# Kernel tuning notes

Hardware: AMD Instinct MI355X
Metric: run time of the kernel (lower is better)

The kernel has to match this reference:

```python
import jax, jax.numpy as jnp
import numpy as np

N = 50000; E = 800000; NFEAT = 128; NHID = 64; CONCAT = 2; NCLASS = 40
D = CONCAT * NHID
BN_EPS = 1e-5


def setup_inputs() -> dict:
    key = jax.random.key(0)
    ks = jax.random.split(key, 16)
    rn = lambda k, s, sc=0.05: jax.random.normal(k, s, jnp.float32) * sc
    return {
        "x1a": rn(ks[0], (N, NFEAT), 1.0),
        "x1b": rn(ks[1], (N, NFEAT), 1.0),
        "x2a": rn(ks[2], (N, NFEAT), 1.0),
        "x2b": rn(ks[3], (N, NFEAT), 1.0),
        "edge_index1": jax.random.randint(ks[4], (2, E), 0, N),
        "edge_index2": jax.random.randint(ks[5], (2, E), 0, N),
        "Wi": rn(ks[6], (CONCAT, NFEAT, NHID)),
        "bi": jnp.zeros((CONCAT, NHID), jnp.float32),
        "gi": jnp.ones((CONCAT, NHID), jnp.float32),
        "bei": jnp.zeros((CONCAT, NHID), jnp.float32),
        "Wm": rn(ks[7], (2, D, D)),
        "bm": jnp.zeros((2, D), jnp.float32),
        "gm": jnp.ones((2, D), jnp.float32),
        "bem": jnp.zeros((2, D), jnp.float32),
        "Wf": rn(ks[8], (D, NCLASS)),
        "bf": jnp.zeros((NCLASS,), jnp.float32),
        "fc1w1_W": rn(ks[9], (D,)),
        "fc1w1_b": jnp.zeros((1,), jnp.float32),
        "fc1w2_W": rn(ks[10], (D,)),
        "fc1w2_b": jnp.zeros((1,), jnp.float32),
        "aws_w1_W": rn(ks[11], (2, D)),
        "aws_w1_b": jnp.zeros((2,), jnp.float32),
        "aws_w2_W": rn(ks[12], (2, D)),
        "aws_w2_b": jnp.zeros((2,), jnp.float32),
        "fcw1_W": rn(ks[13], (NCLASS,)),
        "fcw1_b": jnp.zeros((1,), jnp.float32),
        "fcw2_W": rn(ks[14], (NCLASS,)),
        "fcw2_b": jnp.zeros((1,), jnp.float32),
    }


def _gcn_norm(edge_index, n):
    # GCN symmetric normalization with self-loops (cached=True behaviour)
    loop = jnp.arange(n)
    src = jnp.concatenate([edge_index[0], loop])
    dst = jnp.concatenate([edge_index[1], loop])
    deg = jax.ops.segment_sum(jnp.ones_like(dst, jnp.float32), dst, n)
    dinv = jnp.where(deg > 0, deg ** -0.5, 0.0)
    return src, dst, dinv[src] * dinv[dst]


def _gcn(x, W, b, g):
    # GCNConv: dense projection then sparse scatter-based aggregation
    src, dst, norm = g
    h = x @ W
    agg = jax.ops.segment_sum(h[src] * norm[:, None], dst, x.shape[0])
    return agg + b


def _bn(x, gamma, beta):
    m = x.mean(0)
    v = jnp.mean((x - m) ** 2, axis=0)
    return (x - m) * jax.lax.rsqrt(v + BN_EPS) * gamma + beta


def _gate(x1, x2, w1, b1, w2, b2):
    # sigmoid gates L1-normalized; only the last node's row is used (w[-1,:])
    s1 = jax.nn.sigmoid(jnp.dot(x1[-1], w1) + b1)
    s2 = jax.nn.sigmoid(jnp.dot(x2[-1], w2) + b2)
    t = s1 + s2
    return s1 / t, s2 / t


def _forward(x1a, x1b, x2a, x2b, g1, g2, Wi, bi, gi, bei, Wm, bm, gm, bem,
             Wf, bf, fc1w1_W, fc1w1_b, fc1w2_W, fc1w2_b,
             aws_w1_W, aws_w1_b, aws_w2_W, aws_w2_b,
             fcw1_W, fcw1_b, fcw2_W, fcw2_b):
    xs1, xs2 = (x1a, x1b), (x2a, x2b)
    h1 = jnp.concatenate([jax.nn.relu(_bn(_gcn(xs1[i], Wi[i], bi[i], g1), gi[i], bei[i]))
                          for i in range(CONCAT)], axis=-1)
    h2 = jnp.concatenate([jax.nn.relu(_bn(_gcn(xs2[i], Wi[i], bi[i], g2), gi[i], bei[i]))
                          for i in range(CONCAT)], axis=-1)
    w1, w2 = _gate(h1, h2, fc1w1_W, fc1w1_b[0], fc1w2_W, fc1w2_b[0])
    x = w1 * h1 + w2 * h2
    for i in range(Wm.shape[0]):  # middle layers (n_layers - 2)
        a = jax.nn.relu(_bn(_gcn(x, Wm[i], bm[i], g1), gm[i], bem[i]))
        b = jax.nn.relu(_bn(_gcn(x, Wm[i], bm[i], g2), gm[i], bem[i]))
        w1, w2 = _gate(a, b, aws_w1_W[i], aws_w1_b[i], aws_w2_W[i], aws_w2_b[i])
        x = w1 * a + w2 * b
    p1 = _gcn(x, Wf, bf, g1)
    p2 = _gcn(x, Wf, bf, g2)
    w1, w2 = _gate(p1, p2, fcw1_W, fcw1_b[0], fcw2_W, fcw2_b[0])
    return (w1 * p1 + w2 * p2, p1, p2)


def reference(x1a, x1b, x2a, x2b, edge_index1, edge_index2, Wi, bi, gi, bei,
              Wm, bm, gm, bem, Wf, bf, fc1w1_W, fc1w1_b, fc1w2_W, fc1w2_b,
              aws_w1_W, aws_w1_b, aws_w2_W, aws_w2_b,
              fcw1_W, fcw1_b, fcw2_W, fcw2_b):
    g1 = _gcn_norm(edge_index1, N)
    g2 = _gcn_norm(edge_index2, N)
    return _forward(x1a, x1b, x2a, x2b, g1, g2, Wi, bi, gi, bei, Wm, bm, gm, bem,
                    Wf, bf, fc1w1_W, fc1w1_b, fc1w2_W, fc1w2_b,
                    aws_w1_W, aws_w1_b, aws_w2_W, aws_w2_b,
                    fcw1_W, fcw1_b, fcw2_W, fcw2_b)
```

## Files before the change

### kernel.cpp

```cpp
#include <hip/hip_runtime.h>
#include <hip/hip_fp16.h>


#define DFEAT 128

typedef __attribute__((ext_vector_type(8))) short bf16x8;
typedef __attribute__((ext_vector_type(4))) float f32x4;

__device__ __forceinline__ unsigned short f2bf(float f) {
    unsigned u = __float_as_uint(f);
    u += 0x7fffu + ((u >> 16) & 1u);
    return (unsigned short)(u >> 16);
}
__device__ __forceinline__ float bf2f(unsigned short u) {
    return __uint_as_float((unsigned)u << 16);
}
__device__ __forceinline__ float4 bf4tof4(ushort4 u) {
    return make_float4(__uint_as_float((unsigned)u.x << 16),
                       __uint_as_float((unsigned)u.y << 16),
                       __uint_as_float((unsigned)u.z << 16),
                       __uint_as_float((unsigned)u.w << 16));
}
__device__ __forceinline__ unsigned f2h16(float f) {
    return (unsigned)__half_as_ushort(__float2half(f));
}
__device__ __forceinline__ float h16f(unsigned u) {
    return __half2float(__ushort_as_half((unsigned short)u));
}

constexpr int RSH = 13;
constexpr int RSZ = 8192;
constexpr int NRMAX = 8;
constexpr int EPA = 2048;
constexpr int SUBS = 16;
constexpr int SCAP = 160000;

__global__ __launch_bounds__(256) void partA_kernel(
    const int* __restrict__ src1, const int* __restrict__ dst1,
    const int* __restrict__ src2, const int* __restrict__ dst2,
    int* __restrict__ stg, int* __restrict__ gcount, int E, int nr) {
    int g = blockIdx.y;
    const int* src = g ? src2 : src1;
    const int* dst = g ? dst2 : dst1;
    __shared__ int buf[EPA];
    __shared__ int buf2[EPA];
    __shared__ int cnt8[NRMAX + 1], pre8[NRMAX + 1], base8[NRMAX];
    int t = threadIdx.x;
    if (t < NRMAX) cnt8[t] = 0;
    __syncthreads();
    int e0 = blockIdx.x * EPA;
    int e1 = min(e0 + EPA, E);
    int ec = e1 - e0;
    for (int i = e0 + t; i < e1; i += 256) {
        int d = dst[i];
        int s = src[i];
        buf[i - e0] = (d << 16) | s;
        atomicAdd(&cnt8[d >> RSH], 1);
    }
    __syncthreads();
    if (t == 0) {
        int run = 0;
        for (int r = 0; r < nr; ++r) { pre8[r] = run; run += cnt8[r]; }
        pre8[nr] = run;
    }
    __syncthreads();
    if (t < nr) {
        base8[t] = atomicAdd(&gcount[g * NRMAX + t], cnt8[t]);
        cnt8[t] = 0;
    }
    __syncthreads();
    for (int j = t; j < ec; j += 256) {
        int v = buf[j];
        int d = (unsigned)v >> 16;
        int r = d >> RSH;
        int p = pre8[r] + atomicAdd(&cnt8[r], 1);
        buf2[p] = ((d & (RSZ - 1)) << 16) | (v & 0xFFFF);
    }
    __syncthreads();
    for (int j = t; j < ec; j += 256) {
        int r = 0;
        while (j >= pre8[r + 1]) ++r;
        int gpos = base8[r] + (j - pre8[r]);
        if (gpos < SCAP) stg[((size_t)g * NRMAX + r) * SCAP + gpos] = buf2[j];
    }
}

__global__ __launch_bounds__(256) void histB_kernel(
    const int* __restrict__ stg, const int* __restrict__ gcount,
    int* __restrict__ baseB, int nr) {
    int g = blockIdx.y;
    int r = blockIdx.x / SUBS;
    int sub = blockIdx.x % SUBS;
    __shared__ int hist[RSZ];
    int t = threadIdx.x;
    for (int i = t; i < RSZ; i += 256) hist[i] = 0;
    __syncthreads();
    int len = min(gcount[g * NRMAX + r], SCAP);
    int seg = (len + SUBS - 1) / SUBS;
    int e0 = sub * seg, e1 = min(e0 + seg, len);
    const int* sp = stg + ((size_t)g * NRMAX + r) * SCAP;
    for (int i = e0 + t; i < e1; i += 256) atomicAdd(&hist[(unsigned)sp[i] >> 16], 1);
    __syncthreads();
    int* bp = baseB + (((size_t)(g * NRMAX + r) * SUBS + sub) << RSH);
    for (int i = t; i < RSZ; i += 256) bp[i] = hist[i];
}

__global__ __launch_bounds__(256) void scanB_kernel(
    int* __restrict__ baseB, int* __restrict__ cnt1, int* __restrict__ cnt2, int n) {
    int node = blockIdx.x * 256 + threadIdx.x;
    int g = blockIdx.y;
    if (node >= n) return;
    int r = node >> RSH, dloc = node & (RSZ - 1);
    int* p = baseB + (((size_t)(g * NRMAX + r) * SUBS) << RSH) + dloc;
    int run = 0;
#pragma unroll
    for (int s = 0; s < SUBS; ++s) {
        int v = p[(size_t)s << RSH];
        p[(size_t)s << RSH] = run;
        run += v;
    }
    (g ? cnt2 : cnt1)[node] = run;
}

__global__ __launch_bounds__(256) void fillC_kernel(
    const int* __restrict__ stg, const int* __restrict__ gcount,
    const int* __restrict__ baseB,
    const int* __restrict__ rp1, const int* __restrict__ rp2,
    const float* __restrict__ dv1, const float* __restrict__ dv2,
    int* __restrict__ cs1, int* __restrict__ cs2, int n, int nr) {
    int g = blockIdx.y;
    int r = blockIdx.x / SUBS;
    int sub = blockIdx.x % SUBS;
    const int* rp = g ? rp2 : rp1;
    const float* dv = g ? dv2 : dv1;
    int* cs = g ? cs2 : cs1;
    __shared__ int off[RSZ];
    int t = threadIdx.x;
    int r0 = r << RSH;
    int rn = min(RSZ, n - r0);
    if (rn <= 0) return;
    const int* bp = baseB + (((size_t)(g * NRMAX + r) * SUBS + sub) << RSH);
    for (int i = t; i < rn; i += 256) off[i] = bp[i] + rp[r0 + i];
    __syncthreads();
    int len = min(gcount[g * NRMAX + r], SCAP);
    int seg = (len + SUBS - 1) / SUBS;
    int e0 = sub * seg, e1 = min(e0 + seg, len);
    const int* sp = stg + ((size_t)g * NRMAX + r) * SCAP;
    for (int i = e0 + t; i < e1; i += 256) {
        int v = sp[i];
        int dloc = (unsigned)v >> 16;
        int s = v & 0xFFFF;
        float w = dv[r0 + dloc] * dv[s];
        int pos = atomicAdd(&off[dloc], 1);
        cs[pos] = (int)((f2h16(w) << 16) | (unsigned)s);
    }
}

__global__ __launch_bounds__(256) void blocksum_kernel(const int* __restrict__ c1,
                                                       const int* __restrict__ c2,
                                                       int* __restrict__ bs, int n, int nb) {
    const int* c = blockIdx.y ? c2 : c1;
    int* out = bs + (size_t)blockIdx.y * nb;
    int t = threadIdx.x;
    int base = blockIdx.x * 2048 + t * 8;
    int s = 0;
#pragma unroll
    for (int i = 0; i < 8; ++i) {
        int idx = base + i;
        if (idx < n) s += c[idx];
    }
    __shared__ int red[256];
    red[t] = s;
    __syncthreads();
    for (int o = 128; o > 0; o >>= 1) {
        if (t < o) red[t] += red[t + o];
        __syncthreads();
    }
    if (t == 0) out[blockIdx.x] = red[0];
}

__global__ void scansums_kernel(int* __restrict__ bs, int nb, int* __restrict__ rp1,
                                int* __restrict__ rp2, int n, int E, float* __restrict__ stats) {
    int t = threadIdx.x;
    if (t < 2) {
        int* b = bs + (size_t)t * nb;
        int run = 0;
        for (int i = 0; i < nb; ++i) {
            int v = b[i];
            b[i] = run;
            run += v;
        }
        (t ? rp2 : rp1)[n] = E;
    }
    for (int i = t; i < 512; i += 64) stats[i] = 0.f;
}

__global__ __launch_bounds__(256) void writerp_kernel(const int* __restrict__ c1,
                                                      const int* __restrict__ c2,
                                                      const int* __restrict__ bs,
                                                      int* __restrict__ rp1, int* __restrict__ rp2,
                                                      float* __restrict__ dv1,
                                                      float* __restrict__ dv2, int n, int nb) {
    const int* c = blockIdx.y ? c2 : c1;
    int* rp = blockIdx.y ? rp2 : rp1;
    float* dv = blockIdx.y ? dv2 : dv1;
    int boff = bs[(size_t)blockIdx.y * nb + blockIdx.x];
    int t = threadIdx.x;
    int base = blockIdx.x * 2048 + t * 8;
    int v[8];
    int s = 0;
#pragma unroll
    for (int i = 0; i < 8; ++i) {
        int idx = base + i;
        v[i] = (idx < n) ? c[idx] : 0;
        s += v[i];
    }
    __shared__ int red[256];
    red[t] = s;
    __syncthreads();
    for (int o = 1; o < 256; o <<= 1) {
        int x = (t >= o) ? red[t - o] : 0;
        __syncthreads();
        red[t] += x;
        __syncthreads();
    }
    int run = boff + red[t] - s;
#pragma unroll
    for (int i = 0; i < 8; ++i) {
        int idx = base + i;
        if (idx < n) {
            rp[idx] = run;
            dv[idx] = rsqrtf((float)(v[i] + 1));
            run += v[i];
        }
    }
}

template <int FV, typename OutT>
__global__ __launch_bounds__(256) void dualagg_kernel(
    const unsigned short* __restrict__ h1, const unsigned short* __restrict__ h2,
    const int* __restrict__ rp1, const int* __restrict__ cs1, const float* __restrict__ dv1,
    const int* __restrict__ rp2, const int* __restrict__ cs2, const float* __restrict__ dv2,
    const float* __restrict__ bias, OutT* __restrict__ o1, OutT* __restrict__ o2, int n) {
    constexpr int COLS = FV * 4;
    const unsigned short* h;
    const int *rp, *cs;
    const float* dv;
    OutT* out;
    if (blockIdx.y == 0) { h = h1; rp = rp1; cs = cs1; dv = dv1; out = o1; }
    else                 { h = h2; rp = rp2; cs = cs2; dv = dv2; out = o2; }
    int wid = blockIdx.x * 4 + (threadIdx.x >> 6);
    if (wid >= n) return;
    int lane = threadIdx.x & 63;
    int half = lane >> 5;
    int l = lane & 31;
    bool act = (l < FV);
    float4 acc = make_float4(0.f, 0.f, 0.f, 0.f);
    int e0 = rp[wid], e1 = rp[wid + 1];
    int e = e0 + half;
    for (; e + 6 < e1; e += 8) {
        int va = cs[e], vb = cs[e + 2], vc = cs[e + 4], vd = cs[e + 6];
        float wa = h16f((unsigned)va >> 16); int sa = va & 0xFFFF;
        float wb = h16f((unsigned)vb >> 16); int sb = vb & 0xFFFF;
        float wc = h16f((unsigned)vc >> 16); int sc = vc & 0xFFFF;
        float wd = h16f((unsigned)vd >> 16); int sd = vd & 0xFFFF;
        if (act) {
            float4 ha = bf4tof4(((const ushort4*)(h + (size_t)sa * COLS))[l]);
            float4 hb = bf4tof4(((const ushort4*)(h + (size_t)sb * COLS))[l]);
            float4 hc = bf4tof4(((const ushort4*)(h + (size_t)sc * COLS))[l]);
            float4 hd = bf4tof4(((const ushort4*)(h + (size_t)sd * COLS))[l]);
            acc.x = fmaf(wa, ha.x, acc.x); acc.y = fmaf(wa, ha.y, acc.y);
            acc.z = fmaf(wa, ha.z, acc.z); acc.w = fmaf(wa, ha.w, acc.w);
            acc.x = fmaf(wb, hb.x, acc.x); acc.y = fmaf(wb, hb.y, acc.y);
            acc.z = fmaf(wb, hb.z, acc.z); acc.w = fmaf(wb, hb.w, acc.w);
            acc.x = fmaf(wc, hc.x, acc.x); acc.y = fmaf(wc, hc.y, acc.y);
            acc.z = fmaf(wc, hc.z, acc.z); acc.w = fmaf(wc, hc.w, acc.w);
            acc.x = fmaf(wd, hd.x, acc.x); acc.y = fmaf(wd, hd.y, acc.y);
            acc.z = fmaf(wd, hd.z, acc.z); acc.w = fmaf(wd, hd.w, acc.w);
        }
    }
    for (; e < e1; e += 2) {
        int va = cs[e];
        float wa = h16f((unsigned)va >> 16); int sa = va & 0xFFFF;
        if (act) {
            float4 ha = bf4tof4(((const ushort4*)(h + (size_t)sa * COLS))[l]);
            acc.x = fmaf(wa, ha.x, acc.x); acc.y = fmaf(wa, ha.y, acc.y);
            acc.z = fmaf(wa, ha.z, acc.z); acc.w = fmaf(wa, ha.w, acc.w);
        }
    }
    acc.x += __shfl_xor(acc.x, 32);
    acc.y += __shfl_xor(acc.y, 32);
    acc.z += __shfl_xor(acc.z, 32);
    acc.w += __shfl_xor(acc.w, 32);
    if (half == 0 && act) {
        float dn = dv[wid];
        float w = dn * dn;
        float4 hv = bf4tof4(((const ushort4*)(h + (size_t)wid * COLS))[l]);
        acc.x = fmaf(w, hv.x, acc.x); acc.y = fmaf(w, hv.y, acc.y);
        acc.z = fmaf(w, hv.z, acc.z); acc.w = fmaf(w, hv.w, acc.w);
        float4 b = ((const float4*)bias)[l];
        acc.x += b.x; acc.y += b.y; acc.z += b.z; acc.w += b.w;
        if constexpr (sizeof(OutT) == 4) {
            ((float4*)((float*)out + (size_t)wid * COLS))[l] = acc;
        } else {
            ushort4 o;
            o.x = f2bf(acc.x); o.y = f2bf(acc.y); o.z = f2bf(acc.z); o.w = f2bf(acc.w);
            ((ushort4*)((unsigned short*)out + (size_t)wid * COLS))[l] = o;
        }
    }
}

__global__ __launch_bounds__(256) void prepW1_kernel(const float* __restrict__ Wi,
                                                     unsigned short* __restrict__ Wt1) {
    int o = blockIdx.x * 256 + threadIdx.x;
    int kk = o & 31;
    int col = (o >> 5) & 63;
    int kc = (o >> 11) & 3;
    int h = (o >> 13) & 1;
    int s = (o >> 14) & 1;
    float w = Wi[(size_t)s * 8192 + (size_t)(kc * 32 + kk) * 64 + col];
    unsigned short hi = f2bf(w);
    Wt1[o] = h ? f2bf(w - bf2f(hi)) : hi;
}

__global__ __launch_bounds__(256) void gemm_l1_kernel(
    const float* __restrict__ x1a, const float* __restrict__ x1b, const float* __restrict__ x2a,
    const float* __restrict__ x2b, const unsigned short* __restrict__ Wt1,
    unsigned short* __restrict__ H1, unsigned short* __restrict__ H2, int nrows) {
    const float* X = (blockIdx.y == 0) ? x1a : (blockIdx.y == 1) ? x1b
                     : (blockIdx.y == 2) ? x2a : x2b;
    int slice = blockIdx.y & 1;
    unsigned short* Y = (blockIdx.y < 2) ? H1 : H2;
    int ocol = slice * 64;
    __shared__ unsigned short Xh[64 * 128];
    __shared__ unsigned short Xl[64 * 128];
    int tid = threadIdx.x;
    int row0 = blockIdx.x * 64;
    int wave = tid >> 6, lane = tid & 63;
    int m = lane & 15, quad = lane >> 4;
    for (int u = tid; u < 1024; u += 256) {
        int r = u >> 4;
        int c8 = (u & 15) * 8;
        int sc = c8 ^ ((r & 7) << 3);
        int gr = row0 + r;
        ushort4 h0, h1v, l0, l1v;
        if (gr < nrows) {
            float4 f0 = *(const float4*)(X + (size_t)gr * DFEAT + c8);
            float4 f1 = *(const float4*)(X + (size_t)gr * DFEAT + c8 + 4);
            float fs[8] = {f0.x, f0.y, f0.z, f0.w, f1.x, f1.y, f1.z, f1.w};
            unsigned short hv[8], lv[8];
#pragma unroll
            for (int j = 0; j < 8; ++j) {
                unsigned short hh = f2bf(fs[j]);
                hv[j] = hh;
                lv[j] = f2bf(fs[j] - bf2f(hh));
            }
            h0 = make_ushort4(hv[0], hv[1], hv[2], hv[3]);
            h1v = make_ushort4(hv[4], hv[5], hv[6], hv[7]);
            l0 = make_ushort4(lv[0], lv[1], lv[2], lv[3]);
            l1v = make_ushort4(lv[4], lv[5], lv[6], lv[7]);
        } else {
            h0 = h1v = l0 = l1v = make_ushort4(0, 0, 0, 0);
        }
        *(ushort4*)&Xh[r * 128 + sc] = h0;
        *(ushort4*)&Xh[r * 128 + sc + 4] = h1v;
        *(ushort4*)&Xl[r * 128 + sc] = l0;
        *(ushort4*)&Xl[r * 128 + sc + 4] = l1v;
    }
    __syncthreads();
    f32x4 acc[4];
#pragma unroll
    for (int i = 0; i < 4; ++i) acc[i] = (f32x4){0.f, 0.f, 0.f, 0.f};
    int arow = wave * 16 + m;
    const unsigned short* Whp = Wt1 + (size_t)slice * 16384;
    const unsigned short* Wlp = Whp + 8192;
#pragma unroll
    for (int kc = 0; kc < 4; ++kc) {
        int ac = (kc * 32 + quad * 8) ^ ((arow & 7) << 3);
        bf16x8 ah = *(const bf16x8*)&Xh[arow * 128 + ac];
        bf16x8 al = *(const bf16x8*)&Xl[arow * 128 + ac];
#pragma unroll
        for (int ct = 0; ct < 4; ++ct) {
            int wo = kc * 2048 + (ct * 16 + m) * 32 + quad * 8;
            bf16x8 bh = *(const bf16x8*)(Whp + wo);
            bf16x8 bl = *(const bf16x8*)(Wlp + wo);
            acc[ct] = __builtin_amdgcn_mfma_f32_16x16x32_bf16(ah, bh, acc[ct], 0, 0, 0);
            acc[ct] = __builtin_amdgcn_mfma_f32_16x16x32_bf16(al, bh, acc[ct], 0, 0, 0);
            acc[ct] = __builtin_amdgcn_mfma_f32_16x16x32_bf16(ah, bl, acc[ct], 0, 0, 0);
        }
    }
#pragma unroll
    for (int ct = 0; ct < 4; ++ct) {
#pragma unroll
        for (int i = 0; i < 4; ++i) {
            int gr = row0 + wave * 16 + quad * 4 + i;
            if (gr < nrows) Y[(size_t)gr * DFEAT + ocol + ct * 16 + m] = f2bf(acc[ct][i]);
        }
    }
}

__global__ __launch_bounds__(256) void prepW_kernel(const float* __restrict__ Wm,
                                                    unsigned short* __restrict__ Wt) {
    int o = blockIdx.x * 256 + threadIdx.x;
    int l = blockIdx.y;
    int kk = o & 31;
    int col = (o >> 5) & 127;
    int kc = o >> 12;
    int k = kc * 32 + kk;
    Wt[(size_t)l * 16384 + o] = f2bf(Wm[(size_t)l * 16384 + (size_t)k * 128 + col]);
}

__global__ __launch_bounds__(256) void gemm_mfma_kernel(
    const unsigned short* __restrict__ Abf, const unsigned short* __restrict__ Bbf,
    const float* __restrict__ ss, const float* __restrict__ wout,
    const unsigned short* __restrict__ Wt, unsigned short* __restrict__ Y, int nrows) {
    __shared__ unsigned short Xs[64 * 128];
    int tid = threadIdx.x;
    int row0 = blockIdx.x * 64;
    int wave = tid >> 6, lane = tid & 63;
    int m = lane & 15, quad = lane >> 4;
    float w1 = wout[0], w2 = wout[1];
    for (int u = tid; u < 1024; u += 256) {
        int r = u >> 4;
        int col0 = (u & 15) * 8;
        int gr = row0 + r;
        int swz = (r & 7) << 3;
        if (gr < nrows) {
#pragma unroll
            for (int hh = 0; hh < 2; ++hh) {
                int c = col0 + hh * 4;
                float4 fa = bf4tof4(*(const ushort4*)(Abf + (size_t)gr * 128 + c));
                float4 fb = bf4tof4(*(const ushort4*)(Bbf + (size_t)gr * 128 + c));
                float4 sa = *(const float4*)(ss + c);
                float4 ha = *(const float4*)(ss + 128 + c);
                float4 sb = *(const float4*)(ss + 256 + c);
                float4 hb = *(const float4*)(ss + 384 + c);
                ushort4 o;
                o.x = f2bf(w1 * fmaxf(fmaf(fa.x, sa.x, ha.x), 0.f) +
                           w2 * fmaxf(fmaf(fb.x, sb.x, hb.x), 0.f));
                o.y = f2bf(w1 * fmaxf(fmaf(fa.y, sa.y, ha.y), 0.f) +
                           w2 * fmaxf(fmaf(fb.y, sb.y, hb.y), 0.f));
                o.z = f2bf(w1 * fmaxf(fmaf(fa.z, sa.z, ha.z), 0.f) +
                           w2 * fmaxf(fmaf(fb.z, sb.z, hb.z), 0.f));
                o.w = f2bf(w1 * fmaxf(fmaf(fa.w, sa.w, ha.w), 0.f) +
                           w2 * fmaxf(fmaf(fb.w, sb.w, hb.w), 0.f));
                *(ushort4*)&Xs[r * 128 + (c ^ swz)] = o;
            }
        } else {
            ushort4 z = {0, 0, 0, 0};
            *(ushort4*)&Xs[r * 128 + (col0 ^ swz)] = z;
            *(ushort4*)&Xs[r * 128 + ((col0 + 4) ^ swz)] = z;
        }
    }
    __syncthreads();
    f32x4 acc[8];
#pragma unroll
    for (int i = 0; i < 8; ++i) acc[i] = (f32x4){0.f, 0.f, 0.f, 0.f};
    int arow = wave * 16 + m;
#pragma unroll
    for (int kc = 0; kc < 4; ++kc) {
        int ac = (kc * 32 + quad * 8) ^ ((arow & 7) << 3);
        bf16x8 a = *(const bf16x8*)&Xs[arow * 128 + ac];
#pragma unroll
        for (int ct = 0; ct < 8; ++ct) {
            const unsigned short* bp = Wt + ((size_t)(kc * 128 + ct * 16 + m) * 32) + quad * 8;
            bf16x8 b = *(const bf16x8*)bp;
            acc[ct] = __builtin_amdgcn_mfma_f32_16x16x32_bf16(a, b, acc[ct], 0, 0, 0);
        }
    }
#pragma unroll
    for (int ct = 0; ct < 8; ++ct) {
#pragma unroll
        for (int i = 0; i < 4; ++i) {
            int gr = row0 + wave * 16 + quad * 4 + i;
            if (gr < nrows) Y[(size_t)gr * 128 + ct * 16 + m] = f2bf(acc[ct][i]);
        }
    }
}

template <int CG, int RPT>
__global__ __launch_bounds__(256) void gemm_fused_kernel(
    const unsigned short* __restrict__ Abf, const unsigned short* __restrict__ Bbf,
    const float* __restrict__ ss, const float* __restrict__ wout, const float* __restrict__ W,
    unsigned short* __restrict__ Y, int nrows, int fout, int ostride) {
    __shared__ float Ws[32][CG * 4];
    __shared__ float Xs[64][33];
    int tid = threadIdx.x;
    int row0 = blockIdx.x * 64;
    int cg = tid % CG;
    int rg = tid / CG;
    float w1 = wout[0], w2 = wout[1];
    float4 acc[RPT];
#pragma unroll
    for (int i = 0; i < RPT; ++i) acc[i] = make_float4(0.f, 0.f, 0.f, 0.f);
    for (int kc = 0; kc < 4; ++kc) {
        for (int i = tid; i < 32 * CG; i += 256) {
            int r = i / CG, c = i % CG;
            float4 w;
            if ((c * 4 + 3) < fout) {
                w = *(const float4*)(W + (size_t)(kc * 32 + r) * fout + c * 4);
            } else {
                float t0 = (c * 4 + 0) < fout ? W[(size_t)(kc * 32 + r) * fout + c * 4 + 0] : 0.f;
                float t1 = (c * 4 + 1) < fout ? W[(size_t)(kc * 32 + r) * fout + c * 4 + 1] : 0.f;
                float t2 = (c * 4 + 2) < fout ? W[(size_t)(kc * 32 + r) * fout + c * 4 + 2] : 0.f;
                float t3 = (c * 4 + 3) < fout ? W[(size_t)(kc * 32 + r) * fout + c * 4 + 3] : 0.f;
                w = make_float4(t0, t1, t2, t3);
            }
            *(float4*)&Ws[r][c * 4] = w;
        }
        for (int i = tid; i < 64 * 8; i += 256) {
            int r = i / 8, c = i % 8;
            int gr = row0 + r;
            int col0 = kc * 32 + c * 4;
            float4 v = make_float4(0.f, 0.f, 0.f, 0.f);
            if (gr < nrows) {
                float4 a = bf4tof4(*(const ushort4*)(Abf + (size_t)gr * DFEAT + col0));
                float4 b = bf4tof4(*(const ushort4*)(Bbf + (size_t)gr * DFEAT + col0));
                float4 scA = *(const float4*)(ss + col0);
                float4 shA = *(const float4*)(ss + DFEAT + col0);
                float4 scB = *(const float4*)(ss + 2 * DFEAT + col0);
                float4 shB = *(const float4*)(ss + 3 * DFEAT + col0);
                v.x = w1 * fmaxf(fmaf(a.x, scA.x, shA.x), 0.f) +
                      w2 * fmaxf(fmaf(b.x, scB.x, shB.x), 0.f);
                v.y = w1 * fmaxf(fmaf(a.y, scA.y, shA.y), 0.f) +
                      w2 * fmaxf(fmaf(b.y, scB.y, shB.y), 0.f);
                v.z = w1 * fmaxf(fmaf(a.z, scA.z, shA.z), 0.f) +
                      w2 * fmaxf(fmaf(b.z, scB.z, shB.z), 0.f);
                v.w = w1 * fmaxf(fmaf(a.w, scA.w, shA.w), 0.f) +
                      w2 * fmaxf(fmaf(b.w, scB.w, shB.w), 0.f);
            }
            Xs[r][c * 4 + 0] = v.x;
            Xs[r][c * 4 + 1] = v.y;
            Xs[r][c * 4 + 2] = v.z;
            Xs[r][c * 4 + 3] = v.w;
        }
        __syncthreads();
#pragma unroll
        for (int k = 0; k < 32; ++k) {
            float4 w = *(float4*)&Ws[k][cg * 4];
#pragma unroll
            for (int i = 0; i < RPT; ++i) {
                float a = Xs[rg * RPT + i][k];
                acc[i].x = fmaf(a, w.x, acc[i].x);
                acc[i].y = fmaf(a, w.y, acc[i].y);
                acc[i].z = fmaf(a, w.z, acc[i].z);
                acc[i].w = fmaf(a, w.w, acc[i].w);
            }
        }
        __syncthreads();
    }
    if (cg * 4 < fout) {
#pragma unroll
        for (int i = 0; i < RPT; ++i) {
            int r = row0 + rg * RPT + i;
            if (r < nrows) {
                ushort4 o;
                o.x = f2bf(acc[i].x); o.y = f2bf(acc[i].y);
                o.z = f2bf(acc[i].z); o.w = f2bf(acc[i].w);
                *(ushort4*)(Y + (size_t)r * ostride + cg * 4) = o;
            }
        }
    }
}

__global__ __launch_bounds__(256) void stats2_kernel(const unsigned short* __restrict__ A,
                                                     const unsigned short* __restrict__ B,
                                                     float* __restrict__ stats, int nrows) {
    __shared__ float red1[256];
    __shared__ float red2[256];
    int t = threadIdx.x;
    int col = t & 127;
    int rg = t >> 7;
    const unsigned short* src = (blockIdx.y == 0) ? A : B;
    float* st = stats + (size_t)blockIdx.y * 256;
    int r0 = blockIdx.x * 128 + rg * 64;
    int r1 = min(r0 + 64, nrows);
    float s = 0.f, s2 = 0.f;
    for (int r = r0; r < r1; ++r) {
        float v = bf2f(src[(size_t)r * DFEAT + col]);
        s += v;
        s2 = fmaf(v, v, s2);
    }
    red1[t] = s;
    red2[t] = s2;
    __syncthreads();
    if (t < 128) {
        atomicAdd(&st[col], red1[t] + red1[t + 128]);
        atomicAdd(&st[DFEAT + col], red2[t] + red2[t + 128]);
    }
}

__global__ __launch_bounds__(128) void gate_prep_kernel(
    float* __restrict__ statsA, float* __restrict__ statsB,
    const unsigned short* __restrict__ preA, const unsigned short* __restrict__ preB,
    const float* __restrict__ gamma, const float* __restrict__ beta,
    const float* __restrict__ gwA, const float* __restrict__ gbA,
    const float* __restrict__ gwB, const float* __restrict__ gbB,
    float* __restrict__ ss, float* __restrict__ wout, int nrows) {
    __shared__ float red[128];
    __shared__ float dotA_s;
    int t = threadIdx.x;
    float invN = 1.f / (float)nrows;
    float meanA = statsA[t] * invN;
    float varA = statsA[DFEAT + t] * invN - meanA * meanA;
    float scA = gamma[t] * rsqrtf(varA + 1e-5f);
    float shA = beta[t] - meanA * scA;
    ss[t] = scA;
    ss[DFEAT + t] = shA;
    float meanB = statsB[t] * invN;
    float varB = statsB[DFEAT + t] * invN - meanB * meanB;
    float scB = gamma[t] * rsqrtf(varB + 1e-5f);
    float shB = beta[t] - meanB * scB;
    ss[2 * DFEAT + t] = scB;
    ss[3 * DFEAT + t] = shB;
    statsA[t] = 0.f;
    statsA[DFEAT + t] = 0.f;
    statsB[t] = 0.f;
    statsB[DFEAT + t] = 0.f;
    float av = fmaxf(fmaf(bf2f(preA[(size_t)(nrows - 1) * DFEAT + t]), scA, shA), 0.f);
    red[t] = av * gwA[t];
    __syncthreads();
    for (int s = 64; s > 0; s >>= 1) {
        if (t < s) red[t] += red[t + s];
        __syncthreads();
    }
    if (t == 0) dotA_s = red[0];
    __syncthreads();
    float bv = fmaxf(fmaf(bf2f(preB[(size_t)(nrows - 1) * DFEAT + t]), scB, shB), 0.f);
    red[t] = bv * gwB[t];
    __syncthreads();
    for (int s = 64; s > 0; s >>= 1) {
        if (t < s) red[t] += red[t + s];
        __syncthreads();
    }
    if (t == 0) {
        float s1 = 1.f / (1.f + expf(-(dotA_s + gbA[0])));
        float s2 = 1.f / (1.f + expf(-(red[0] + gbB[0])));
        float tt = s1 + s2;
        wout[0] = s1 / tt;
        wout[1] = s2 / tt;
    }
}

__global__ __launch_bounds__(64) void gate_final_kernel(
    const float* __restrict__ p1, const float* __restrict__ p2,
    const float* __restrict__ w1v, const float* __restrict__ b1,
    const float* __restrict__ w2v, const float* __restrict__ b2,
    float* __restrict__ wout, int nrows, int nclass) {
    __shared__ float red[64];
    __shared__ float dot1_s;
    int t = threadIdx.x;
    float v = (t < nclass) ? p1[(size_t)(nrows - 1) * nclass + t] * w1v[t] : 0.f;
    red[t] = v;
    __syncthreads();
    for (int s = 32; s > 0; s >>= 1) {
        if (t < s) red[t] += red[t + s];
        __syncthreads();
    }
    if (t == 0) dot1_s = red[0];
    __syncthreads();
    v = (t < nclass) ? p2[(size_t)(nrows - 1) * nclass + t] * w2v[t] : 0.f;
    red[t] = v;
    __syncthreads();
    for (int s = 32; s > 0; s >>= 1) {
        if (t < s) red[t] += red[t + s];
        __syncthreads();
    }
    if (t == 0) {
        float s1 = 1.f / (1.f + expf(-(dot1_s + b1[0])));
        float s2 = 1.f / (1.f + expf(-(red[0] + b2[0])));
        float tt = s1 + s2;
        wout[0] = s1 / tt;
        wout[1] = s2 / tt;
    }
}

__global__ __launch_bounds__(256) void mix_kernel(const float* __restrict__ p1,
                                                  const float* __restrict__ p2,
                                                  const float* __restrict__ wout,
                                                  float* __restrict__ o, int n4) {
    int idx = blockIdx.x * blockDim.x + threadIdx.x;
    if (idx >= n4) return;
    float w1 = wout[0], w2 = wout[1];
    float4 a = *(const float4*)(p1 + (size_t)idx * 4);
    float4 b = *(const float4*)(p2 + (size_t)idx * 4);
    float4 r = make_float4(w1 * a.x + w2 * b.x, w1 * a.y + w2 * b.y, w1 * a.z + w2 * b.z,
                           w1 * a.w + w2 * b.w);
    *(float4*)(o + (size_t)idx * 4) = r;
}

extern "C" void kernel_launch(void* const* d_in, const int* in_sizes, int n_in, void* d_out,
                              int out_size, void* d_ws, size_t ws_size, hipStream_t stream) {
    (void)n_in; (void)out_size; (void)ws_size;
    const int N = in_sizes[0] / DFEAT;
    const int E = in_sizes[4] / 2;
    const int NC = in_sizes[15];

    const float* x1a = (const float*)d_in[0];
    const float* x1b = (const float*)d_in[1];
    const float* x2a = (const float*)d_in[2];
    const float* x2b = (const float*)d_in[3];
    const int* ei1 = (const int*)d_in[4];
    const int* ei2 = (const int*)d_in[5];
    const float* Wi = (const float*)d_in[6];
    const float* bi = (const float*)d_in[7];
    const float* gi = (const float*)d_in[8];
    const float* bei = (const float*)d_in[9];
    const float* Wm = (const float*)d_in[10];
    const float* bm = (const float*)d_in[11];
    const float* gm = (const float*)d_in[12];
    const float* bem = (const float*)d_in[13];
    const float* Wf = (const float*)d_in[14];
    const float* bf = (const float*)d_in[15];
    const float* fc1w1_W = (const float*)d_in[16];
    const float* fc1w1_b = (const float*)d_in[17];
    const float* fc1w2_W = (const float*)d_in[18];
    const float* fc1w2_b = (const float*)d_in[19];
    const float* aws_w1_W = (const float*)d_in[20];
    const float* aws_w1_b = (const float*)d_in[21];
    const float* aws_w2_W = (const float*)d_in[22];
    const float* aws_w2_b = (const float*)d_in[23];
    const float* fcw1_W = (const float*)d_in[24];
    const float* fcw1_b = (const float*)d_in[25];
    const float* fcw2_W = (const float*)d_in[26];
    const float* fcw2_b = (const float*)d_in[27];

    char* ws = (char*)d_ws;
    size_t off = 0;
    auto alloc = [&](size_t bytes) -> char* {
        char* p = ws + off;
        off += (bytes + 255) & ~(size_t)255;
        return p;
    };
    unsigned short* A = (unsigned short*)alloc((size_t)N * DFEAT * 2);
    unsigned short* B = (unsigned short*)alloc((size_t)N * DFEAT * 2);
    unsigned short* H1 = (unsigned short*)alloc((size_t)N * DFEAT * 2);
    unsigned short* H2 = (unsigned short*)alloc((size_t)N * DFEAT * 2);
    int* rp1 = (int*)alloc((size_t)(N + 1) * 4);
    int* rp2 = (int*)alloc((size_t)(N + 1) * 4);
    int* cnt1 = (int*)alloc((size_t)N * 4);
    int* cnt2 = (int*)alloc((size_t)N * 4);
    float* dv1 = (float*)alloc((size_t)N * 4);
    float* dv2 = (float*)alloc((size_t)N * 4);
    int* cs1 = (int*)alloc((size_t)E * 4);
    int* cs2 = (int*)alloc((size_t)E * 4);
    int* stg = (int*)alloc((size_t)2 * NRMAX * SCAP * 4);
    int* baseB = (int*)alloc(((size_t)2 * NRMAX * SUBS << RSH) * 4);
    int* gcount = (int*)alloc(2 * NRMAX * 4);
    unsigned short* Wt = (unsigned short*)alloc((size_t)2 * 16384 * 2);
    unsigned short* Wt1 = (unsigned short*)alloc((size_t)32768 * 2);
    float* stats = (float*)alloc(2048);
    float* statsA = stats;
    float* statsB = stats + 256;
    float* ssbuf = (float*)alloc(2048);
    float* wout = (float*)alloc(256);
    int nb = (N + 2047) / 2048;
    int* bsums = (int*)alloc((size_t)2 * nb * 4);

    const int* src1 = ei1;
    const int* dst1 = ei1 + E;
    const int* src2 = ei2;
    const int* dst2 = ei2 + E;

    int nr = (N + RSZ - 1) >> RSH;
    int gemmbl = (N + 63) / 64;
    dim3 pagrid((E + EPA - 1) / EPA, 2);
    dim3 rsgrid(nr * SUBS, 2);
    dim3 ssgrid((N + 255) / 256, 2);
    dim3 agggrid((N + 3) / 4, 2);
    dim3 statgrid((N + 127) / 128, 2);
    dim3 scangrid(nb, 2);
    dim3 l1grid(gemmbl, 4);
    dim3 prepgrid(64, 2);

    hipMemsetAsync(gcount, 0, 2 * NRMAX * 4, stream);
    prepW_kernel<<<prepgrid, 256, 0, stream>>>(Wm, Wt);
    prepW1_kernel<<<128, 256, 0, stream>>>(Wi, Wt1);
    partA_kernel<<<pagrid, 256, 0, stream>>>(src1, dst1, src2, dst2, stg, gcount, E, nr);
    histB_kernel<<<rsgrid, 256, 0, stream>>>(stg, gcount, baseB, nr);
    scanB_kernel<<<ssgrid, 256, 0, stream>>>(baseB, cnt1, cnt2, N);
    blocksum_kernel<<<scangrid, 256, 0, stream>>>(cnt1, cnt2, bsums, N, nb);
    scansums_kernel<<<1, 64, 0, stream>>>(bsums, nb, rp1, rp2, N, E, stats);
    writerp_kernel<<<scangrid, 256, 0, stream>>>(cnt1, cnt2, bsums, rp1, rp2, dv1, dv2, N, nb);
    fillC_kernel<<<rsgrid, 256, 0, stream>>>(stg, gcount, baseB, rp1, rp2, dv1, dv2,
                                             cs1, cs2, N, nr);

    gemm_l1_kernel<<<l1grid, 256, 0, stream>>>(x1a, x1b, x2a, x2b, Wt1, H1, H2, N);
    dualagg_kernel<32, unsigned short><<<agggrid, 256, 0, stream>>>(
        H1, H2, rp1, cs1, dv1, rp2, cs2, dv2, bi, A, B, N);
    stats2_kernel<<<statgrid, 256, 0, stream>>>(A, B, stats, N);
    gate_prep_kernel<<<1, 128, 0, stream>>>(statsA, statsB, A, B, gi, bei, fc1w1_W, fc1w1_b,
                                            fc1w2_W, fc1w2_b, ssbuf, wout, N);

    gemm_mfma_kernel<<<gemmbl, 256, 0, stream>>>(A, B, ssbuf, wout, Wt, H1, N);
    dualagg_kernel<32, unsigned short><<<agggrid, 256, 0, stream>>>(
        H1, H1, rp1, cs1, dv1, rp2, cs2, dv2, bm, A, B, N);
    stats2_kernel<<<statgrid, 256, 0, stream>>>(A, B, stats, N);
    gate_prep_kernel<<<1, 128, 0, stream>>>(statsA, statsB, A, B, gm, bem, aws_w1_W, aws_w1_b,
                                            aws_w2_W, aws_w2_b, ssbuf, wout, N);

    gemm_mfma_kernel<<<gemmbl, 256, 0, stream>>>(A, B, ssbuf, wout, Wt + 16384, H1, N);
    dualagg_kernel<32, unsigned short><<<agggrid, 256, 0, stream>>>(
        H1, H1, rp1, cs1, dv1, rp2, cs2, dv2, bm + 128, A, B, N);
    stats2_kernel<<<statgrid, 256, 0, stream>>>(A, B, stats, N);
    gate_prep_kernel<<<1, 128, 0, stream>>>(statsA, statsB, A, B, gm + 128, bem + 128,
                                            aws_w1_W + 128, aws_w1_b + 1, aws_w2_W + 128,
                                            aws_w2_b + 1, ssbuf, wout, N);

    float* out0 = (float*)d_out;
    float* p1 = out0 + (size_t)N * NC;
    float* p2 = out0 + (size_t)2 * N * NC;
    gemm_fused_kernel<16, 4><<<gemmbl, 256, 0, stream>>>(A, B, ssbuf, wout, Wf, H2, N, NC, NC);
    dualagg_kernel<10, float><<<agggrid, 256, 0, stream>>>(H2, H2, rp1, cs1, dv1, rp2, cs2, dv2,
                                                           bf, p1, p2, N);
    gate_final_kernel<<<1, 64, 0, stream>>>(p1, p2, fcw1_W, fcw1_b, fcw2_W, fcw2_b, wout, N, NC);
    mix_kernel<<<(N * NC / 4 + 255) / 256, 256, 0, stream>>>(p1, p2, wout, out0, N * NC / 4);
}
```

Baseline: 694.0 us.

## Widen aggregation gathers to 16-byte loads and drop LDS staging in layer-1 GEMM

The dual aggregation kernel now splits each wave into four 16-lane groups. Each lane gathers 8 bf16 features with one 16-byte load, and the partial sums are reduced across groups with two xor shuffles. Each edge row is fetched with fewer, wider load instructions and 8 rows stay in flight, at the cost of more accumulator registers and an extra shuffle stage. Separately, the layer-1 GEMM no longer stages the bf16 hi/lo split of X in shared memory. Each lane loads its A fragment straight from global memory and splits it in registers, which removes the LDS traffic and the barrier but makes the global reads less coalesced.

```diff
diff --git a/kernel.cpp b/kernel.cpp
--- a/kernel.cpp
+++ b/kernel.cpp
@@ -14,6 +14,12 @@
 }
 __device__ __forceinline__ float bf2f(unsigned short u) {
     return __uint_as_float((unsigned)u << 16);
+}
+__device__ __forceinline__ unsigned f2h16(float f) {
+    return (unsigned)__half_as_ushort(__float2half(f));
+}
+__device__ __forceinline__ float h16f(unsigned u) {
+    return __half2float(__ushort_as_half((unsigned short)u));
 }
 __device__ __forceinline__ float4 bf4tof4(ushort4 u) {
     return make_float4(__uint_as_float((unsigned)u.x << 16),
@@ -21,11 +27,15 @@
                        __uint_as_float((unsigned)u.z << 16),
                        __uint_as_float((unsigned)u.w << 16));
 }
-__device__ __forceinline__ unsigned f2h16(float f) {
-    return (unsigned)__half_as_ushort(__float2half(f));
-}
-__device__ __forceinline__ float h16f(unsigned u) {
-    return __half2float(__ushort_as_half((unsigned short)u));
+__device__ __forceinline__ void acc8(float* acc, float w, int4 r) {
+    int vs[4] = {r.x, r.y, r.z, r.w};
+#pragma unroll
+    for (int q = 0; q < 4; ++q) {
+        float lo = __uint_as_float((unsigned)vs[q] << 16);
+        float hi = __uint_as_float((unsigned)vs[q] & 0xffff0000u);
+        acc[q * 2] = fmaf(w, lo, acc[q * 2]);
+        acc[q * 2 + 1] = fmaf(w, hi, acc[q * 2 + 1]);
+    }
 }
 
 constexpr int RSH = 13;
@@ -236,13 +246,13 @@
     }
 }
 
-template <int FV, typename OutT>
+template <int COLS, typename OutT>
 __global__ __launch_bounds__(256) void dualagg_kernel(
     const unsigned short* __restrict__ h1, const unsigned short* __restrict__ h2,
     const int* __restrict__ rp1, const int* __restrict__ cs1, const float* __restrict__ dv1,
     const int* __restrict__ rp2, const int* __restrict__ cs2, const float* __restrict__ dv2,
     const float* __restrict__ bias, OutT* __restrict__ o1, OutT* __restrict__ o2, int n) {
-    constexpr int COLS = FV * 4;
+    constexpr int ACT = COLS / 8;
     const unsigned short* h;
     const int *rp, *cs;
     const float* dv;
@@ -252,60 +262,56 @@
     int wid = blockIdx.x * 4 + (threadIdx.x >> 6);
     if (wid >= n) return;
     int lane = threadIdx.x & 63;
-    int half = lane >> 5;
-    int l = lane & 31;
-    bool act = (l < FV);
-    float4 acc = make_float4(0.f, 0.f, 0.f, 0.f);
+    int grp = lane >> 4;
+    int li = lane & 15;
+    bool act = li < ACT;
+    float acc[8] = {0.f, 0.f, 0.f, 0.f, 0.f, 0.f, 0.f, 0.f};
     int e0 = rp[wid], e1 = rp[wid + 1];
-    int e = e0 + half;
-    for (; e + 6 < e1; e += 8) {
-        int va = cs[e], vb = cs[e + 2], vc = cs[e + 4], vd = cs[e + 6];
+    int e = e0 + grp;
+    for (; e + 4 < e1; e += 8) {
+        int va = cs[e], vb = cs[e + 4];
         float wa = h16f((unsigned)va >> 16); int sa = va & 0xFFFF;
         float wb = h16f((unsigned)vb >> 16); int sb = vb & 0xFFFF;
-        float wc = h16f((unsigned)vc >> 16); int sc = vc & 0xFFFF;
-        float wd = h16f((unsigned)vd >> 16); int sd = vd & 0xFFFF;
         if (act) {
-            float4 ha = bf4tof4(((const ushort4*)(h + (size_t)sa * COLS))[l]);
-            float4 hb = bf4tof4(((const ushort4*)(h + (size_t)sb * COLS))[l]);
-            float4 hc = bf4tof4(((const ushort4*)(h + (size_t)sc * COLS))[l]);
-            float4 hd = bf4tof4(((const ushort4*)(h + (size_t)sd * COLS))[l]);
-            acc.x = fmaf(wa, ha.x, acc.x); acc.y = fmaf(wa, ha.y, acc.y);
-            acc.z = fmaf(wa, ha.z, acc.z); acc.w = fmaf(wa, ha.w, acc.w);
-            acc.x = fmaf(wb, hb.x, acc.x); acc.y = fmaf(wb, hb.y, acc.y);
-            acc.z = fmaf(wb, hb.z, acc.z); acc.w = fmaf(wb, hb.w, acc.w);
-            acc.x = fmaf(wc, hc.x, acc.x); acc.y = fmaf(wc, hc.y, acc.y);
-            acc.z = fmaf(wc, hc.z, acc.z); acc.w = fmaf(wc, hc.w, acc.w);
-            acc.x = fmaf(wd, hd.x, acc.x); acc.y = fmaf(wd, hd.y, acc.y);
-            acc.z = fmaf(wd, hd.z, acc.z); acc.w = fmaf(wd, hd.w, acc.w);
-        }
-    }
-    for (; e < e1; e += 2) {
+            int4 ra = *(const int4*)(h + (size_t)sa * COLS + li * 8);
+            int4 rb = *(const int4*)(h + (size_t)sb * COLS + li * 8);
+            acc8(acc, wa, ra);
+            acc8(acc, wb, rb);
+        }
+    }
+    if (e < e1) {
         int va = cs[e];
         float wa = h16f((unsigned)va >> 16); int sa = va & 0xFFFF;
         if (act) {
-            float4 ha = bf4tof4(((const ushort4*)(h + (size_t)sa * COLS))[l]);
-            acc.x = fmaf(wa, ha.x, acc.x); acc.y = fmaf(wa, ha.y, acc.y);
-            acc.z = fmaf(wa, ha.z, acc.z); acc.w = fmaf(wa, ha.w, acc.w);
-        }
-    }
-    acc.x += __shfl_xor(acc.x, 32);
-    acc.y += __shfl_xor(acc.y, 32);
-    acc.z += __shfl_xor(acc.z, 32);
-    acc.w += __shfl_xor(acc.w, 32);
-    if (half == 0 && act) {
+            int4 ra = *(const int4*)(h + (size_t)sa * COLS + li * 8);
+            acc8(acc, wa, ra);
+        }
+    }
+#pragma unroll
+    for (int j = 0; j < 8; ++j) {
+        acc[j] += __shfl_xor(acc[j], 16);
+        acc[j] += __shfl_xor(acc[j], 32);
+    }
+    if (grp == 0 && act) {
         float dn = dv[wid];
         float w = dn * dn;
-        float4 hv = bf4tof4(((const ushort4*)(h + (size_t)wid * COLS))[l]);
-        acc.x = fmaf(w, hv.x, acc.x); acc.y = fmaf(w, hv.y, acc.y);
-        acc.z = fmaf(w, hv.z, acc.z); acc.w = fmaf(w, hv.w, acc.w);
-        float4 b = ((const float4*)bias)[l];
-        acc.x += b.x; acc.y += b.y; acc.z += b.z; acc.w += b.w;
+        int4 rs = *(const int4*)(h + (size_t)wid * COLS + li * 8);
+        acc8(acc, w, rs);
+        float4 b0 = ((const float4*)bias)[li * 2];
+        float4 b1 = ((const float4*)bias)[li * 2 + 1];
+        acc[0] += b0.x; acc[1] += b0.y; acc[2] += b0.z; acc[3] += b0.w;
+        acc[4] += b1.x; acc[5] += b1.y; acc[6] += b1.z; acc[7] += b1.w;
         if constexpr (sizeof(OutT) == 4) {
-            ((float4*)((float*)out + (size_t)wid * COLS))[l] = acc;
+            float* op = (float*)out + (size_t)wid * COLS + li * 8;
+            *(float4*)op = make_float4(acc[0], acc[1], acc[2], acc[3]);
+            *(float4*)(op + 4) = make_float4(acc[4], acc[5], acc[6], acc[7]);
         } else {
-            ushort4 o;
-            o.x = f2bf(acc.x); o.y = f2bf(acc.y); o.z = f2bf(acc.z); o.w = f2bf(acc.w);
-            ((ushort4*)((unsigned short*)out + (size_t)wid * COLS))[l] = o;
+            int4 o;
+            o.x = (int)((unsigned)f2bf(acc[0]) | ((unsigned)f2bf(acc[1]) << 16));
+            o.y = (int)((unsigned)f2bf(acc[2]) | ((unsigned)f2bf(acc[3]) << 16));
+            o.z = (int)((unsigned)f2bf(acc[4]) | ((unsigned)f2bf(acc[5]) << 16));
+            o.w = (int)((unsigned)f2bf(acc[6]) | ((unsigned)f2bf(acc[7]) << 16));
+            *(int4*)((unsigned short*)out + (size_t)wid * COLS + li * 8) = o;
         }
     }
 }
@@ -332,53 +338,34 @@
     int slice = blockIdx.y & 1;
     unsigned short* Y = (blockIdx.y < 2) ? H1 : H2;
     int ocol = slice * 64;
-    __shared__ unsigned short Xh[64 * 128];
-    __shared__ unsigned short Xl[64 * 128];
     int tid = threadIdx.x;
     int row0 = blockIdx.x * 64;
     int wave = tid >> 6, lane = tid & 63;
     int m = lane & 15, quad = lane >> 4;
-    for (int u = tid; u < 1024; u += 256) {
-        int r = u >> 4;
-        int c8 = (u & 15) * 8;
-        int sc = c8 ^ ((r & 7) << 3);
-        int gr = row0 + r;
-        ushort4 h0, h1v, l0, l1v;
-        if (gr < nrows) {
-            float4 f0 = *(const float4*)(X + (size_t)gr * DFEAT + c8);
-            float4 f1 = *(const float4*)(X + (size_t)gr * DFEAT + c8 + 4);
-            float fs[8] = {f0.x, f0.y, f0.z, f0.w, f1.x, f1.y, f1.z, f1.w};
-            unsigned short hv[8], lv[8];
-#pragma unroll
-            for (int j = 0; j < 8; ++j) {
-                unsigned short hh = f2bf(fs[j]);
-                hv[j] = hh;
-                lv[j] = f2bf(fs[j] - bf2f(hh));
-            }
-            h0 = make_ushort4(hv[0], hv[1], hv[2], hv[3]);
-            h1v = make_ushort4(hv[4], hv[5], hv[6], hv[7]);
-            l0 = make_ushort4(lv[0], lv[1], lv[2], lv[3]);
-            l1v = make_ushort4(lv[4], lv[5], lv[6], lv[7]);
-        } else {
-            h0 = h1v = l0 = l1v = make_ushort4(0, 0, 0, 0);
-        }
-        *(ushort4*)&Xh[r * 128 + sc] = h0;
-        *(ushort4*)&Xh[r * 128 + sc + 4] = h1v;
-        *(ushort4*)&Xl[r * 128 + sc] = l0;
-        *(ushort4*)&Xl[r * 128 + sc + 4] = l1v;
-    }
-    __syncthreads();
-    f32x4 acc[4];
-#pragma unroll
-    for (int i = 0; i < 4; ++i) acc[i] = (f32x4){0.f, 0.f, 0.f, 0.f};
-    int arow = wave * 16 + m;
+    int arow = row0 + wave * 16 + m;
+    bool rv = arow < nrows;
+    const float* xp = X + (size_t)arow * DFEAT;
     const unsigned short* Whp = Wt1 + (size_t)slice * 16384;
     const unsigned short* Wlp = Whp + 8192;
+    f32x4 acc[4];
+#pragma unroll
+    for (int i = 0; i < 4; ++i) acc[i] = (f32x4){0.f, 0.f, 0.f, 0.f};
 #pragma unroll
     for (int kc = 0; kc < 4; ++kc) {
-        int ac = (kc * 32 + quad * 8) ^ ((arow & 7) << 3);
-        bf16x8 ah = *(const bf16x8*)&Xh[arow * 128 + ac];
-        bf16x8 al = *(const bf16x8*)&Xl[arow * 128 + ac];
+        float4 f0 = make_float4(0.f, 0.f, 0.f, 0.f);
+        float4 f1 = make_float4(0.f, 0.f, 0.f, 0.f);
+        if (rv) {
+            f0 = *(const float4*)(xp + kc * 32 + quad * 8);
+            f1 = *(const float4*)(xp + kc * 32 + quad * 8 + 4);
+        }
+        float fs[8] = {f0.x, f0.y, f0.z, f0.w, f1.x, f1.y, f1.z, f1.w};
+        bf16x8 ah, al;
+#pragma unroll
+        for (int j = 0; j < 8; ++j) {
+            unsigned short hh = f2bf(fs[j]);
+            ah[j] = (short)hh;
+            al[j] = (short)f2bf(fs[j] - bf2f(hh));
+        }
 #pragma unroll
         for (int ct = 0; ct < 4; ++ct) {
             int wo = kc * 2048 + (ct * 16 + m) * 32 + quad * 8;
@@ -786,21 +773,21 @@
                                              cs1, cs2, N, nr);
 
     gemm_l1_kernel<<<l1grid, 256, 0, stream>>>(x1a, x1b, x2a, x2b, Wt1, H1, H2, N);
-    dualagg_kernel<32, unsigned short><<<agggrid, 256, 0, stream>>>(
+    dualagg_kernel<128, unsigned short><<<agggrid, 256, 0, stream>>>(
         H1, H2, rp1, cs1, dv1, rp2, cs2, dv2, bi, A, B, N);
     stats2_kernel<<<statgrid, 256, 0, stream>>>(A, B, stats, N);
     gate_prep_kernel<<<1, 128, 0, stream>>>(statsA, statsB, A, B, gi, bei, fc1w1_W, fc1w1_b,
                                             fc1w2_W, fc1w2_b, ssbuf, wout, N);
 
     gemm_mfma_kernel<<<gemmbl, 256, 0, stream>>>(A, B, ssbuf, wout, Wt, H1, N);
-    dualagg_kernel<32, unsigned short><<<agggrid, 256, 0, stream>>>(
+    dualagg_kernel<128, unsigned short><<<agggrid, 256, 0, stream>>>(
         H1, H1, rp1, cs1, dv1, rp2, cs2, dv2, bm, A, B, N);
     stats2_kernel<<<statgrid, 256, 0, stream>>>(A, B, stats, N);
     gate_prep_kernel<<<1, 128, 0, stream>>>(statsA, statsB, A, B, gm, bem, aws_w1_W, aws_w1_b,
                                             aws_w2_W, aws_w2_b, ssbuf, wout, N);
 
     gemm_mfma_kernel<<<gemmbl, 256, 0, stream>>>(A, B, ssbuf, wout, Wt + 16384, H1, N);
-    dualagg_kernel<32, unsigned short><<<agggrid, 256, 0, stream>>>(
+    dualagg_kernel<128, unsigned short><<<agggrid, 256, 0, stream>>>(
         H1, H1, rp1, cs1, dv1, rp2, cs2, dv2, bm + 128, A, B, N);
     stats2_kernel<<<statgrid, 256, 0, stream>>>(A, B, stats, N);
     gate_prep_kernel<<<1, 128, 0, stream>>>(statsA, statsB, A, B, gm + 128, bem + 128,
@@ -811,7 +798,7 @@
     float* p1 = out0 + (size_t)N * NC;
     float* p2 = out0 + (size_t)2 * N * NC;
     gemm_fused_kernel<16, 4><<<gemmbl, 256, 0, stream>>>(A, B, ssbuf, wout, Wf, H2, N, NC, NC);
-    dualagg_kernel<10, float><<<agggrid, 256, 0, stream>>>(H2, H2, rp1, cs1, dv1, rp2, cs2, dv2,
+    dualagg_kernel<40, float><<<agggrid, 256, 0, stream>>>(H2, H2, rp1, cs1, dv1, rp2, cs2, dv2,
                                                            bf, p1, p2, N);
     gate_final_kernel<<<1, 64, 0, stream>>>(p1, p2, fcw1_W, fcw1_b, fcw2_W, fcw2_b, wout, N, NC);
     mix_kernel<<<(N * NC / 4 + 255) / 256, 256, 0, stream>>>(p1, p2, wout, out0, N * NC / 4);
```

Result: faster. 668.6 us (-3.7%).
